# Kernel optimization log

Measured on AMD Instinct MI355X. Metric: run time of the kernel, lower is better.

Reference implementation:

```python
import jax, jax.numpy as jnp
import numpy as np

NEG = -1e30  # finite stand-in for -inf in the sparse-softmax mask


def setup_inputs() -> dict:
    key = jax.random.key(0)
    kh, kwl, kwn, kn = jax.random.split(key, 4)
    B, S, D, E = 8, 4096, 1024, 64
    return {
        "h": jax.random.normal(kh, (B, S, D), dtype=jnp.float32),
        "Wl": jax.random.normal(kwl, (E, D), dtype=jnp.float32) * 0.02,
        "bl": jnp.zeros((E,), dtype=jnp.float32),
        "Wn": jax.random.normal(kwn, (E, D), dtype=jnp.float32) * 0.02,
        "bn": jnp.zeros((E,), dtype=jnp.float32),
        "noise": jax.random.normal(kn, (B, S, E), dtype=jnp.float32),
        "top_k": 2,
    }


def reference(h, Wl, bl, Wn, bn, noise, top_k):
    # logits, noise std: two small linears over the expert dim
    logits = jnp.einsum("bsd,ed->bse", h, Wl) + bl          # [B,S,E]
    std = jax.nn.softplus(jnp.einsum("bsd,ed->bse", h, Wn) + bn)
    noisy = logits + noise * std                              # [B,S,E]

    full_p = jax.nn.softmax(noisy, axis=-1)

    topk_vals, ix = jax.lax.top_k(noisy, top_k)               # [B,S,k]
    E = noisy.shape[-1]
    # scatter top-k values back into a -inf-filled tensor == mask non-topk
    mask = jax.nn.one_hot(ix, E, dtype=jnp.bool_).any(axis=-2)  # [B,S,E]
    sparse = jnp.where(mask, noisy, NEG)
    route_p = jax.nn.softmax(sparse, axis=-1)
    return route_p, ix, full_p
```

## Files before the change

### kernel.cpp

```cpp
#include <hip/hip_runtime.h>
#include <math.h>


#define DIM 1024
#define NEXP 64
#define LS 40
#define CS 132
#define HALF_BUF 15360
#define A_LO 2560
#define B_HI 5120
#define B_LO 10240
#define LOSCALE 2048.0f
#define INV_LOSCALE (1.0f / 2048.0f)

using half4v   = __attribute__((ext_vector_type(4)))  _Float16;
using half8v   = __attribute__((ext_vector_type(8)))  _Float16;
using floatx16 = __attribute__((ext_vector_type(16))) float;

__device__ inline void split4(const float4 v, half4v& hi, half4v& lo) {
    _Float16 h0 = (_Float16)v.x, h1 = (_Float16)v.y,
             h2 = (_Float16)v.z, h3 = (_Float16)v.w;
    hi = (half4v){h0, h1, h2, h3};
    lo = (half4v){(_Float16)((v.x - (float)h0) * LOSCALE),
                  (_Float16)((v.y - (float)h1) * LOSCALE),
                  (_Float16)((v.z - (float)h2) * LOSCALE),
                  (_Float16)((v.w - (float)h3) * LOSCALE)};
}

#define MFMA32(a, b, c) __builtin_amdgcn_mfma_f32_32x32x16_f16((a), (b), (c), 0, 0, 0)

__global__ __launch_bounds__(512, 4)
void router_fused(const float* __restrict__ h,  const float* __restrict__ Wl,
                  const float* __restrict__ bl, const float* __restrict__ Wn,
                  const float* __restrict__ bn, const float* __restrict__ noise,
                  float* __restrict__ outR, float* __restrict__ outIx,
                  float* __restrict__ outF, int M)
{
    __shared__ _Float16 lds[2 * HALF_BUF];

    const int tid   = threadIdx.x;
    const int wv    = tid >> 6;
    const int lane  = tid & 63;
    const int row31 = lane & 31;
    const int oct   = lane >> 5;
    const int tokg  = (wv >> 2) * 32;
    const int expg  = (wv & 3) * 32;
    const int tok0  = blockIdx.x * 64;

    const int srow = tid >> 3;
    const int skq  = tid & 7;
    const float* hp  = h  + (size_t)(tok0 + srow) * DIM + skq * 4;
    const float* wp0 = Wl + (size_t)srow * DIM + skq * 4;
    const float* wp1 = Wn + (size_t)srow * DIM + skq * 4;
    const int sA  = srow * LS + skq * 4;
    const int sB0 = B_HI + srow * LS + skq * 4;
    const int sB1 = B_HI + (srow + 64) * LS + skq * 4;

    const int aoffs = (tokg + row31) * LS + oct * 8;
    const int boffs = (expg + row31) * LS + oct * 8;

    floatx16 acc1, acc2;
#pragma unroll
    for (int i = 0; i < 16; i++) { acc1[i] = 0.f; acc2[i] = 0.f; }

    float4 av  = *(const float4*)(hp);
    float4 bv0 = *(const float4*)(wp0);
    float4 bv1 = *(const float4*)(wp1);
    {
        half4v hi, lo;
        split4(av, hi, lo);
        *(half4v*)(lds + sA) = hi;        *(half4v*)(lds + A_LO + sA) = lo;
        split4(bv0, hi, lo);
        *(half4v*)(lds + sB0) = hi;       *(half4v*)(lds + B_LO - B_HI + sB0) = lo;
        split4(bv1, hi, lo);
        *(half4v*)(lds + sB1) = hi;       *(half4v*)(lds + B_LO - B_HI + sB1) = lo;
    }
    av  = *(const float4*)(hp + 32);
    bv0 = *(const float4*)(wp0 + 32);
    bv1 = *(const float4*)(wp1 + 32);
    __syncthreads();

    for (int t = 0; t < 32; t++) {
        if (t < 31) {
            _Float16* bufS = lds + ((t + 1) & 1) * HALF_BUF;
            half4v hi, lo;
            split4(av, hi, lo);
            *(half4v*)(bufS + sA) = hi;   *(half4v*)(bufS + A_LO + sA) = lo;
            split4(bv0, hi, lo);
            *(half4v*)(bufS + sB0) = hi;  *(half4v*)(bufS + B_LO - B_HI + sB0) = lo;
            split4(bv1, hi, lo);
            *(half4v*)(bufS + sB1) = hi;  *(half4v*)(bufS + B_LO - B_HI + sB1) = lo;
        }
        if (t < 30) {
            av  = *(const float4*)(hp  + 32 * (t + 2));
            bv0 = *(const float4*)(wp0 + 32 * (t + 2));
            bv1 = *(const float4*)(wp1 + 32 * (t + 2));
        }
        {
            const _Float16* bufC = lds + (t & 1) * HALF_BUF;
#pragma unroll
            for (int ks = 0; ks < 2; ks++) {
                half8v aH = *(const half8v*)(bufC + aoffs + ks * 16);
                half8v aL = *(const half8v*)(bufC + A_LO + aoffs + ks * 16);
                half8v bH = *(const half8v*)(bufC + B_HI + boffs + ks * 16);
                half8v bL = *(const half8v*)(bufC + B_LO + boffs + ks * 16);
                acc1 = MFMA32(aH, bH, acc1);
                acc2 = MFMA32(aH, bL, acc2);
                acc2 = MFMA32(aL, bH, acc2);
            }
        }
        __syncthreads();
    }

    float* Cs = (float*)lds;
#pragma unroll
    for (int i = 0; i < 16; i++) {
        int rowt = (i & 3) + 8 * (i >> 2) + 4 * oct;
        Cs[(tokg + rowt) * CS + expg + row31] = acc1[i] + acc2[i] * INV_LOSCALE;
    }
    __syncthreads();

    const float blv = bl[lane];
    const float bnv = bn[lane];

    for (int t = wv; t < 64; t += 8) {
        const int gt = tok0 + t;
        float xr = Cs[t * CS + lane] + blv;
        float xf = Cs[t * CS + 64 + lane] + bnv;
        float nz = noise[(size_t)gt * NEXP + lane];

        float stdv = fmaxf(xf, 0.f) + log1pf(expf(-fabsf(xf)));
        float noisy = fmaf(nz, stdv, xr);

        float m = noisy;
#pragma unroll
        for (int o = 32; o > 0; o >>= 1) m = fmaxf(m, __shfl_xor(m, o, 64));
        float p = expf(noisy - m);
        float s = p;
#pragma unroll
        for (int o = 32; o > 0; o >>= 1) s += __shfl_xor(s, o, 64);
        float fullp = p / s;

        float v = noisy; int idx = lane;
#pragma unroll
        for (int o = 32; o > 0; o >>= 1) {
            float ov = __shfl_xor(v, o, 64);
            int   oi = __shfl_xor(idx, o, 64);
            if (ov > v || (ov == v && oi < idx)) { v = ov; idx = oi; }
        }
        const float v1 = v; const int i1 = idx;
        v = (lane == i1) ? -INFINITY : noisy; idx = lane;
#pragma unroll
        for (int o = 32; o > 0; o >>= 1) {
            float ov = __shfl_xor(v, o, 64);
            int   oi = __shfl_xor(idx, o, 64);
            if (ov > v || (ov == v && oi < idx)) { v = ov; idx = oi; }
        }
        const float v2 = v; const int i2 = idx;

        float e2 = expf(v2 - v1);
        float den = 1.f + e2;
        float routep = (lane == i1) ? (1.f / den) : ((lane == i2) ? (e2 / den) : 0.f);

        outR[(size_t)gt * NEXP + lane] = routep;
        outF[(size_t)gt * NEXP + lane] = fullp;
        if (lane == 0) {
            outIx[(size_t)gt * 2 + 0] = (float)i1;
            outIx[(size_t)gt * 2 + 1] = (float)i2;
        }
    }
}

extern "C" void kernel_launch(void* const* d_in, const int* in_sizes, int n_in,
                              void* d_out, int out_size, void* d_ws, size_t ws_size,
                              hipStream_t stream) {
    const float* h     = (const float*)d_in[0];
    const float* Wl    = (const float*)d_in[1];
    const float* bl    = (const float*)d_in[2];
    const float* Wn    = (const float*)d_in[3];
    const float* bn    = (const float*)d_in[4];
    const float* noise = (const float*)d_in[5];
    float* out = (float*)d_out;

    const int M = in_sizes[0] / DIM;
    float* outR  = out;
    float* outIx = out + (size_t)M * NEXP;
    float* outF  = outIx + (size_t)M * 2;

    router_fused<<<M / 64, 512, 0, stream>>>(h, Wl, bl, Wn, bn, noise,
                                             outR, outIx, outF, M);
}
```

Measured before the change: 239.4 us.

## Presplit weights into fp16 fragment layout and split-K across two waves

A small pre-kernel splits the two weight matrices into hi/lo fp16 halves once and stores them in MFMA fragment order in workspace. The main kernel then reads B fragments straight from global/L2 instead of re-splitting and staging weights through LDS in every block. Each 128-thread block handles 32 tokens with split-K across its two waves, and the partial sums are combined through shared memory. This removes per-block weight conversion and most barriers, at the cost of an extra launch and heavy global B traffic served from cache.

```diff
diff --git a/kernel.cpp b/kernel.cpp
--- a/kernel.cpp
+++ b/kernel.cpp
@@ -6,10 +6,6 @@
 #define NEXP 64
 #define LS 40
 #define CS 132
-#define HALF_BUF 15360
-#define A_LO 2560
-#define B_HI 5120
-#define B_LO 10240
 #define LOSCALE 2048.0f
 #define INV_LOSCALE (1.0f / 2048.0f)
 
@@ -27,106 +23,128 @@
                   (_Float16)((v.w - (float)h3) * LOSCALE)};
 }
 
+__device__ inline half8v mk8(const half4v a, const half4v b) {
+    return (half8v){a[0], a[1], a[2], a[3], b[0], b[1], b[2], b[3]};
+}
+
 #define MFMA32(a, b, c) __builtin_amdgcn_mfma_f32_32x32x16_f16((a), (b), (c), 0, 0, 0)
 
-__global__ __launch_bounds__(512, 4)
-void router_fused(const float* __restrict__ h,  const float* __restrict__ Wl,
-                  const float* __restrict__ bl, const float* __restrict__ Wn,
-                  const float* __restrict__ bn, const float* __restrict__ noise,
-                  float* __restrict__ outR, float* __restrict__ outIx,
-                  float* __restrict__ outF, int M)
+__global__ __launch_bounds__(64)
+void split_B(const float* __restrict__ Wl, const float* __restrict__ Wn,
+             _Float16* __restrict__ bhi, _Float16* __restrict__ blo)
 {
-    __shared__ _Float16 lds[2 * HALF_BUF];
+    const int g = blockIdx.x * 64 + threadIdx.x;
+    const int lane = g & 63;
+    const int f    = (g >> 6) & 63;
+    const int nc   = g >> 12;
+    const int e = nc * 32 + (lane & 31);
+    const int k = f * 16 + (lane >> 5) * 8;
+    const float* W = ((e < NEXP) ? (Wl + (size_t)e * DIM)
+                                 : (Wn + (size_t)(e - NEXP) * DIM)) + k;
+    float4 v0 = *(const float4*)(W);
+    float4 v1 = *(const float4*)(W + 4);
+    half4v h0, l0, h1, l1;
+    split4(v0, h0, l0);
+    split4(v1, h1, l1);
+    *(half8v*)(bhi + (size_t)g * 8) = mk8(h0, h1);
+    *(half8v*)(blo + (size_t)g * 8) = mk8(l0, l1);
+}
+
+__global__ __launch_bounds__(128, 2)
+void router_main(const float* __restrict__ h, const _Float16* __restrict__ bhi,
+                 const _Float16* __restrict__ blo, const float* __restrict__ bl,
+                 const float* __restrict__ bn, const float* __restrict__ noise,
+                 float* __restrict__ outR, float* __restrict__ outIx,
+                 float* __restrict__ outF, int M)
+{
+    __shared__ float smem[2 * 32 * CS];
 
     const int tid   = threadIdx.x;
     const int wv    = tid >> 6;
     const int lane  = tid & 63;
     const int row31 = lane & 31;
     const int oct   = lane >> 5;
-    const int tokg  = (wv >> 2) * 32;
-    const int expg  = (wv & 3) * 32;
-    const int tok0  = blockIdx.x * 64;
-
-    const int srow = tid >> 3;
-    const int skq  = tid & 7;
-    const float* hp  = h  + (size_t)(tok0 + srow) * DIM + skq * 4;
-    const float* wp0 = Wl + (size_t)srow * DIM + skq * 4;
-    const float* wp1 = Wn + (size_t)srow * DIM + skq * 4;
-    const int sA  = srow * LS + skq * 4;
-    const int sB0 = B_HI + srow * LS + skq * 4;
-    const int sB1 = B_HI + (srow + 64) * LS + skq * 4;
-
-    const int aoffs = (tokg + row31) * LS + oct * 8;
-    const int boffs = (expg + row31) * LS + oct * 8;
-
-    floatx16 acc1, acc2;
-#pragma unroll
-    for (int i = 0; i < 16; i++) { acc1[i] = 0.f; acc2[i] = 0.f; }
-
-    float4 av  = *(const float4*)(hp);
-    float4 bv0 = *(const float4*)(wp0);
-    float4 bv1 = *(const float4*)(wp1);
-    {
-        half4v hi, lo;
-        split4(av, hi, lo);
-        *(half4v*)(lds + sA) = hi;        *(half4v*)(lds + A_LO + sA) = lo;
-        split4(bv0, hi, lo);
-        *(half4v*)(lds + sB0) = hi;       *(half4v*)(lds + B_LO - B_HI + sB0) = lo;
-        split4(bv1, hi, lo);
-        *(half4v*)(lds + sB1) = hi;       *(half4v*)(lds + B_LO - B_HI + sB1) = lo;
+    const int tok0  = blockIdx.x * 32;
+    const int kbase = wv * 512;
+
+    _Float16* Abase = (_Float16*)smem + wv * 5120;
+
+    const int arow = lane >> 1, acol = lane & 1;
+    const float* hp = h + (size_t)(tok0 + arow) * DIM + kbase + acol * 16;
+    const int sA = arow * LS + acol * 16;
+    const int fA = row31 * LS + oct * 8;
+
+    const _Float16* bhp = bhi + (size_t)lane * 8 + (size_t)(wv * 16) * 2 * 512;
+    const _Float16* blp = blo + (size_t)lane * 8 + (size_t)(wv * 16) * 2 * 512;
+
+    floatx16 acc1[4], acc2[4];
+#pragma unroll
+    for (int nc = 0; nc < 4; nc++)
+#pragma unroll
+        for (int i = 0; i < 16; i++) { acc1[nc][i] = 0.f; acc2[nc][i] = 0.f; }
+
+    float4 av[4];
+#pragma unroll
+    for (int q = 0; q < 4; q++) av[q] = *(const float4*)(hp + q * 4);
+
+    for (int t = 0; t < 16; t++) {
+        _Float16* Ahi = Abase + (t & 1) * 2560;
+        _Float16* Alo = Ahi + 1280;
+#pragma unroll
+        for (int q = 0; q < 4; q++) {
+            half4v hi, lo;
+            split4(av[q], hi, lo);
+            *(half4v*)(Ahi + sA + q * 4) = hi;
+            *(half4v*)(Alo + sA + q * 4) = lo;
+        }
+        half8v aH[2], aL[2];
+#pragma unroll
+        for (int ks = 0; ks < 2; ks++) {
+            aH[ks] = *(const half8v*)(Ahi + fA + ks * 16);
+            aL[ks] = *(const half8v*)(Alo + fA + ks * 16);
+        }
+        if (t < 15) {
+#pragma unroll
+            for (int q = 0; q < 4; q++)
+                av[q] = *(const float4*)(hp + (t + 1) * 32 + q * 4);
+        }
+#pragma unroll
+        for (int nc = 0; nc < 4; nc++) {
+#pragma unroll
+            for (int ks = 0; ks < 2; ks++) {
+                const size_t off = (size_t)(nc * 64 + t * 2 + ks) * 512;
+                half8v bH = *(const half8v*)(bhp + off);
+                half8v bL = *(const half8v*)(blp + off);
+                acc1[nc] = MFMA32(aH[ks], bH, acc1[nc]);
+                acc2[nc] = MFMA32(aH[ks], bL, acc2[nc]);
+                acc2[nc] = MFMA32(aL[ks], bH, acc2[nc]);
+            }
+        }
     }
-    av  = *(const float4*)(hp + 32);
-    bv0 = *(const float4*)(wp0 + 32);
-    bv1 = *(const float4*)(wp1 + 32);
+
     __syncthreads();
 
-    for (int t = 0; t < 32; t++) {
-        if (t < 31) {
-            _Float16* bufS = lds + ((t + 1) & 1) * HALF_BUF;
-            half4v hi, lo;
-            split4(av, hi, lo);
-            *(half4v*)(bufS + sA) = hi;   *(half4v*)(bufS + A_LO + sA) = lo;
-            split4(bv0, hi, lo);
-            *(half4v*)(bufS + sB0) = hi;  *(half4v*)(bufS + B_LO - B_HI + sB0) = lo;
-            split4(bv1, hi, lo);
-            *(half4v*)(bufS + sB1) = hi;  *(half4v*)(bufS + B_LO - B_HI + sB1) = lo;
-        }
-        if (t < 30) {
-            av  = *(const float4*)(hp  + 32 * (t + 2));
-            bv0 = *(const float4*)(wp0 + 32 * (t + 2));
-            bv1 = *(const float4*)(wp1 + 32 * (t + 2));
-        }
-        {
-            const _Float16* bufC = lds + (t & 1) * HALF_BUF;
-#pragma unroll
-            for (int ks = 0; ks < 2; ks++) {
-                half8v aH = *(const half8v*)(bufC + aoffs + ks * 16);
-                half8v aL = *(const half8v*)(bufC + A_LO + aoffs + ks * 16);
-                half8v bH = *(const half8v*)(bufC + B_HI + boffs + ks * 16);
-                half8v bL = *(const half8v*)(bufC + B_LO + boffs + ks * 16);
-                acc1 = MFMA32(aH, bH, acc1);
-                acc2 = MFMA32(aH, bL, acc2);
-                acc2 = MFMA32(aL, bH, acc2);
-            }
-        }
-        __syncthreads();
-    }
-
-    float* Cs = (float*)lds;
-#pragma unroll
-    for (int i = 0; i < 16; i++) {
-        int rowt = (i & 3) + 8 * (i >> 2) + 4 * oct;
-        Cs[(tokg + rowt) * CS + expg + row31] = acc1[i] + acc2[i] * INV_LOSCALE;
+    float* Cs = smem + wv * (32 * CS);
+#pragma unroll
+    for (int nc = 0; nc < 4; nc++) {
+#pragma unroll
+        for (int i = 0; i < 16; i++) {
+            int rowt = (i & 3) + 8 * (i >> 2) + 4 * oct;
+            Cs[rowt * CS + nc * 32 + row31] = acc1[nc][i] + acc2[nc][i] * INV_LOSCALE;
+        }
     }
     __syncthreads();
 
     const float blv = bl[lane];
     const float bnv = bn[lane];
-
-    for (int t = wv; t < 64; t += 8) {
+    const float* Cs0 = smem;
+    const float* Cs1 = smem + 32 * CS;
+
+    for (int i = 0; i < 16; i++) {
+        const int t = wv * 16 + i;
         const int gt = tok0 + t;
-        float xr = Cs[t * CS + lane] + blv;
-        float xf = Cs[t * CS + 64 + lane] + bnv;
+        float xr = Cs0[t * CS + lane] + Cs1[t * CS + lane] + blv;
+        float xf = Cs0[t * CS + 64 + lane] + Cs1[t * CS + 64 + lane] + bnv;
         float nz = noise[(size_t)gt * NEXP + lane];
 
         float stdv = fmaxf(xf, 0.f) + log1pf(expf(-fabsf(xf)));
@@ -187,6 +205,10 @@
     float* outIx = out + (size_t)M * NEXP;
     float* outF  = outIx + (size_t)M * 2;
 
-    router_fused<<<M / 64, 512, 0, stream>>>(h, Wl, bl, Wn, bn, noise,
-                                             outR, outIx, outF, M);
-}
+    _Float16* bhi = (_Float16*)d_ws;
+    _Float16* blo = bhi + 128 * DIM;
+
+    split_B<<<256, 64, 0, stream>>>(Wl, Wn, bhi, blo);
+    router_main<<<M / 32, 128, 0, stream>>>(h, bhi, blo, bl, bn, noise,
+                                            outR, outIx, outF, M);
+}
```

Result: slower. 259.5 us (+8.4%).
